# Kernel tuning notes

Measured on AMD Instinct MI355X. Metric: run time of the kernel, lower is better.

## Reference

```python
import jax, jax.numpy as jnp
import numpy as np
from jax import lax

DIM = 96
D_STATE = 16
D_CONV = 4
EXPAND = 2
D_INNER = EXPAND * DIM           # 192
DT_RANK = (DIM + 15) // 16       # 6
EPS = 1e-5


def _upsample2x_align_corners(x):
    # bilinear, align_corners=True, scale_factor=2 (matches nn.Upsample)
    B, C, H, W = x.shape
    def lin_idx(n_in, n_out):
        pos = jnp.arange(n_out) * ((n_in - 1) / (n_out - 1))
        i0 = jnp.floor(pos).astype(jnp.int32)
        i1 = jnp.minimum(i0 + 1, n_in - 1)
        w = (pos - i0).astype(x.dtype)
        return i0, i1, w
    r0, r1, rw = lin_idx(H, 2 * H)
    c0, c1, cw = lin_idx(W, 2 * W)
    xr = x[:, :, r0, :] * (1 - rw)[None, None, :, None] + x[:, :, r1, :] * rw[None, None, :, None]
    return xr[:, :, :, c0] * (1 - cw) + xr[:, :, :, c1] * cw


def _conv2d(x, w, b, pad):
    y = lax.conv_general_dilated(x, w, (1, 1), [(pad, pad), (pad, pad)],
                                 dimension_numbers=('NCHW', 'OIHW', 'NCHW'))
    return y + b[None, :, None, None]


def _instance_norm(x):
    m = x.mean(axis=(2, 3), keepdims=True)
    v = x.var(axis=(2, 3), keepdims=True)
    return (x - m) * lax.rsqrt(v + EPS)


def _selective_scan(u, dt, A, Bm, Cm, D):
    # u, dt: [B,L,Din]; Bm, Cm: [B,L,N]; A: [Din,N]; D: [Din]
    def step(h, inp):
        u_t, dt_t, B_t, C_t = inp                       # [B,Din],[B,Din],[B,N],[B,N]
        dA = jnp.exp(dt_t[..., None] * A)               # [B,Din,N]
        h = h * dA + (dt_t * u_t)[..., None] * B_t[:, None, :]
        y = jnp.einsum('bdn,bn->bd', h, C_t)
        return h, y
    Bsz, L, Din = u.shape
    h0 = jnp.zeros((Bsz, Din, A.shape[1]), u.dtype)
    xs = (u.swapaxes(0, 1), dt.swapaxes(0, 1), Bm.swapaxes(0, 1), Cm.swapaxes(0, 1))
    _, ys = lax.scan(step, h0, xs)                      # ys: [L,B,Din]
    return ys.swapaxes(0, 1) + u * D


def _mamba(xseq, in_proj_w, conv1d_w, conv1d_b, x_proj_w, dt_proj_w, dt_proj_b,
           A_log, D, out_proj_w):
    # xseq: [B,L,dim]
    xz = xseq @ in_proj_w.T                             # [B,L,2*Din]
    xin, z = jnp.split(xz, 2, axis=-1)
    xc = xin.swapaxes(1, 2)                             # [B,Din,L]
    xc = lax.conv_general_dilated(xc, conv1d_w, (1,), [(D_CONV - 1, 0)],
                                  dimension_numbers=('NCH', 'OIH', 'NCH'),
                                  feature_group_count=D_INNER)
    xc = xc + conv1d_b[None, :, None]
    u = jax.nn.silu(xc.swapaxes(1, 2))                  # [B,L,Din]
    x_dbl = u @ x_proj_w.T                              # [B,L,dt_rank+2N]
    dt, Bm, Cm = jnp.split(x_dbl, [DT_RANK, DT_RANK + D_STATE], axis=-1)
    dt = jax.nn.softplus(dt @ dt_proj_w.T + dt_proj_b)  # [B,L,Din]
    A = -jnp.exp(A_log)                                 # [Din,N]
    y = _selective_scan(u, dt, A, Bm, Cm, D)
    y = y * jax.nn.silu(z)
    return y @ out_proj_w.T                             # [B,L,dim]


def setup_inputs() -> dict:
    key = jax.random.key(0)
    ks = jax.random.split(key, 16)
    s = 0.05
    inp = {
        'x': jax.random.normal(ks[0], (2, DIM, 64, 64), jnp.float32),
        'Hx': jax.random.normal(ks[1], (2, DIM * 2, 128, 128), jnp.float32),
        'conv1_w': jax.random.normal(ks[2], (DIM, DIM * 3, 1, 1), jnp.float32) * s,
        'conv1_b': jax.random.normal(ks[3], (DIM,), jnp.float32) * s,
        'conv2_w': jax.random.normal(ks[4], (DIM, DIM, 3, 3), jnp.float32) * s,
        'conv2_b': jax.random.normal(ks[5], (DIM,), jnp.float32) * s,
        'conv3_w': jax.random.normal(ks[6], (DIM, DIM, 1, 1), jnp.float32) * s,
        'conv3_b': jax.random.normal(ks[7], (DIM,), jnp.float32) * s,
        'in_proj_w': jax.random.normal(ks[8], (2 * D_INNER, DIM), jnp.float32) * s,
        'conv1d_w': jax.random.normal(ks[9], (D_INNER, 1, D_CONV), jnp.float32) * s,
        'conv1d_b': jax.random.normal(ks[10], (D_INNER,), jnp.float32) * s,
        'x_proj_w': jax.random.normal(ks[11], (DT_RANK + 2 * D_STATE, D_INNER), jnp.float32) * s,
        'dt_proj_w': jax.random.normal(ks[12], (D_INNER, DT_RANK), jnp.float32) * s,
        'dt_proj_b': jax.random.normal(ks[13], (D_INNER,), jnp.float32) * 0.1,
        'A_log': jnp.log(jnp.tile(jnp.arange(1, D_STATE + 1, dtype=jnp.float32)[None, :], (D_INNER, 1))),
        'D': jnp.ones((D_INNER,), jnp.float32),
        'out_proj_w': jax.random.normal(ks[14], (DIM, D_INNER), jnp.float32) * s,
    }
    return inp


def reference(x, Hx, conv1_w, conv1_b, conv2_w, conv2_b, conv3_w, conv3_b,
              in_proj_w, conv1d_w, conv1d_b, x_proj_w, dt_proj_w, dt_proj_b,
              A_log, D, out_proj_w):
    up = _upsample2x_align_corners(x)                   # [B,dim,H,W]
    cat = jnp.concatenate([up, Hx], axis=1)             # [B,3*dim,H,W]
    h = _conv2d(cat, conv1_w, conv1_b, 0)
    h = _conv2d(h, conv2_w, conv2_b, 1)
    h = _conv2d(h, conv3_w, conv3_b, 0)
    Lx = jax.nn.selu(_instance_norm(h))                 # [B,dim,H,W]
    B, C, H, W = Lx.shape
    seq = Lx.reshape(B, C, H * W).swapaxes(1, 2)        # [B,L,dim]
    y = _mamba(seq, in_proj_w, conv1d_w, conv1d_b, x_proj_w, dt_proj_w,
               dt_proj_b, A_log, D, out_proj_w)
    return y.swapaxes(1, 2).reshape(B, C, H, W) + Lx
```

## Files before the change

kernel.cpp:

```cpp
#include <hip/hip_runtime.h>
#include <hip/hip_bf16.h>
#include <math.h>

#define LSEQ 16384
#define DIN  192
#define GCH  256
#define TCH  64

typedef float f4v __attribute__((ext_vector_type(4)));
typedef short s8v __attribute__((ext_vector_type(8)));
typedef unsigned short u16x8 __attribute__((ext_vector_type(8)));

__device__ __forceinline__ float siluf(float x) { return x / (1.0f + __expf(-x)); }
__device__ __forceinline__ unsigned short f2bf(float f) {
  unsigned int u = __float_as_uint(f);
  unsigned int r = (u + 0x7FFFu + ((u >> 16) & 1u)) >> 16;
  return (unsigned short)r;
}
__device__ __forceinline__ float bf2f(unsigned short s) {
  return __uint_as_float(((unsigned int)s) << 16);
}

__global__ __launch_bounds__(256) void k_packw(const float* __restrict__ c1w,
    const float* __restrict__ c2w, const float* __restrict__ c3w,
    const float* __restrict__ Win, const float* __restrict__ Wx,
    const float* __restrict__ Wout, unsigned short* __restrict__ P) {
  int i = blockIdx.x * 256 + threadIdx.x;
  if (i >= 184320) return;
  if (i < 27648) { P[i] = f2bf(c1w[i]); return; }
  int j = i - 27648;
  if (j < 82944) {
    int cc = j / 27648, r = j - cc * 27648;
    int kk = r / 3072, r2 = r - kk * 3072;
    int oc = r2 >> 5, icl = r2 & 31;
    int ky = kk / 3, kx = kk - ky * 3;
    P[i] = f2bf(c2w[((oc * 96 + cc * 32 + icl) * 3 + ky) * 3 + kx]);
    return;
  }
  j -= 82944;
  if (j < 9216) { P[i] = f2bf(c3w[j]); return; }
  j -= 9216;
  if (j < 36864) { P[i] = f2bf(Win[j]); return; }
  j -= 36864;
  if (j < 9216) {
    int oc = j / 192, k = j - oc * 192;
    P[i] = (oc < 38) ? f2bf(Wx[oc * 192 + k]) : (unsigned short)0;
    return;
  }
  j -= 9216;
  P[i] = f2bf(Wout[j]);
}

__global__ __launch_bounds__(256) void k_upsample(const float* __restrict__ x, float* __restrict__ up) {
  int idx = blockIdx.x * 256 + threadIdx.x;
  if (idx >= 2 * 96 * LSEQ) return;
  int ow = idx & 127, oh = (idx >> 7) & 127, bc = idx >> 14;
  float pr = oh * (63.0f / 127.0f); int r0 = (int)pr; float rw = pr - (float)r0; int r1 = min(r0 + 1, 63);
  float pc = ow * (63.0f / 127.0f); int c0 = (int)pc; float cw = pc - (float)c0; int c1 = min(c0 + 1, 63);
  const float* xp = x + (size_t)bc * 4096;
  float v00 = xp[r0 * 64 + c0], v01 = xp[r0 * 64 + c1];
  float v10 = xp[r1 * 64 + c0], v11 = xp[r1 * 64 + c1];
  float top = v00 + (v10 - v00) * rw;
  float bot = v01 + (v11 - v01) * rw;
  up[idx] = top + (bot - top) * cw;
}

#define SRC_PLANAR2 0
#define SRC_ROWS    1
#define OUT_BF16R    0
#define OUT_F32P     1
#define OUT_F32R     2
#define OUT_BF16RG   3
#define OUT_F32P_RES 4

template<int SM, int OM, int NT>
__global__ __launch_bounds__(256) void k_gemm(
    const void* __restrict__ xa, const void* __restrict__ xb, int CA,
    const unsigned short* __restrict__ Wp, const float* __restrict__ bias,
    void* __restrict__ outv, const float* __restrict__ resid,
    int K, int ostride, int oc0g, int ng) {
  __shared__ unsigned short x_t[128 * 96];
  __shared__ unsigned short w_t[NT * 16 * 96];
  Wp += (size_t)blockIdx.y * 96 * K;
  oc0g += blockIdx.y * 96;
  int pxg0 = blockIdx.x * 128;
  int b = pxg0 >> 14, px_in0 = pxg0 & 16383;
  int tid = threadIdx.x, lane = tid & 63, wv = tid >> 6;
  int r = lane & 15, q = lane >> 4;
  f4v acc[2][NT];
#pragma unroll
  for (int mi = 0; mi < 2; mi++)
#pragma unroll
    for (int n = 0; n < NT; n++) acc[mi][n] = (f4v)0.0f;
  int nchunk = K / 96;
  for (int kc = 0; kc < nchunk; kc++) {
    for (int t = tid; t < NT * 16 * 12; t += 256) {
      int row = t / 12, u8 = t - row * 12;
      *(u16x8*)&w_t[row * 96 + u8 * 8] = *(const u16x8*)&Wp[(size_t)row * K + kc * 96 + u8 * 8];
    }
    if (SM == SRC_PLANAR2) {
      const float* A0 = (const float*)xa;
      const float* A1 = (const float*)xb;
      int CB = K - CA;
      for (int t = tid; t < 3072; t += 256) {
        int px4 = t / 96, c_l = t - px4 * 96;
        int c = kc * 96 + c_l;
        const float* sp = (c < CA) ? (A0 + ((size_t)b * CA + c) * LSEQ + px_in0 + px4 * 4)
                                   : (A1 + ((size_t)b * CB + (c - CA)) * LSEQ + px_in0 + px4 * 4);
        float4 v = *(const float4*)sp;
        x_t[(px4 * 4 + 0) * 96 + c_l] = f2bf(v.x);
        x_t[(px4 * 4 + 1) * 96 + c_l] = f2bf(v.y);
        x_t[(px4 * 4 + 2) * 96 + c_l] = f2bf(v.z);
        x_t[(px4 * 4 + 3) * 96 + c_l] = f2bf(v.w);
      }
    } else {
      const unsigned short* X = (const unsigned short*)xa;
      for (int t = tid; t < 1536; t += 256) {
        int rr = t / 12, u8 = t - rr * 12;
        *(u16x8*)&x_t[rr * 96 + u8 * 8] =
            *(const u16x8*)&X[(size_t)(pxg0 + rr) * K + kc * 96 + u8 * 8];
      }
    }
    __syncthreads();
#pragma unroll
    for (int k0 = 0; k0 < 96; k0 += 32) {
      s8v a0 = *(const s8v*)&x_t[((wv * 2 + 0) * 16 + r) * 96 + k0 + q * 8];
      s8v a1 = *(const s8v*)&x_t[((wv * 2 + 1) * 16 + r) * 96 + k0 + q * 8];
#pragma unroll
      for (int n = 0; n < NT; n++) {
        s8v bb = *(const s8v*)&w_t[(n * 16 + r) * 96 + k0 + q * 8];
        acc[0][n] = __builtin_amdgcn_mfma_f32_16x16x32_bf16(a0, bb, acc[0][n], 0, 0, 0);
        acc[1][n] = __builtin_amdgcn_mfma_f32_16x16x32_bf16(a1, bb, acc[1][n], 0, 0, 0);
      }
    }
    __syncthreads();
  }
#pragma unroll
  for (int mi = 0; mi < 2; mi++) {
    int pxl = (wv * 2 + mi) * 16 + q * 4;
    int pxg = pxg0 + pxl;
#pragma unroll
    for (int n = 0; n < NT; n++) {
      int oc = n * 16 + r;
      if (OM == OUT_BF16R) {
        float bv = bias[oc];
        unsigned short* O = (unsigned short*)outv;
#pragma unroll
        for (int g = 0; g < 4; g++)
          O[(size_t)(pxg + g) * 96 + oc] = f2bf(acc[mi][n][g] + bv);
      } else if (OM == OUT_F32P) {
        float bv = bias[oc];
        float* O = (float*)outv;
        float4 o = make_float4(acc[mi][n][0] + bv, acc[mi][n][1] + bv,
                               acc[mi][n][2] + bv, acc[mi][n][3] + bv);
        *(float4*)&O[((size_t)b * 96 + oc) * LSEQ + px_in0 + pxl] = o;
      } else if (OM == OUT_F32P_RES) {
        float* O = (float*)outv;
        size_t ad = ((size_t)b * 96 + oc) * LSEQ + px_in0 + pxl;
        float4 rv = *(const float4*)&resid[ad];
        float4 o = make_float4(acc[mi][n][0] + rv.x, acc[mi][n][1] + rv.y,
                               acc[mi][n][2] + rv.z, acc[mi][n][3] + rv.w);
        *(float4*)&O[ad] = o;
      } else if (OM == OUT_F32R) {
        float* O = (float*)outv;
        int ocg = oc0g + oc;
        if (ocg < ng) {
#pragma unroll
          for (int g = 0; g < 4; g++)
            O[(size_t)(pxg + g) * ostride + ocg] = acc[mi][n][g];
        }
      } else {
        unsigned short* O = (unsigned short*)outv;
        int ocg = oc0g + oc;
#pragma unroll
        for (int g = 0; g < 4; g++)
          O[(size_t)(pxg + g) * ostride + ocg] = f2bf(acc[mi][n][g]);
      }
    }
  }
}

__global__ __launch_bounds__(256) void k_conv3x3m(const unsigned short* __restrict__ X,
    const unsigned short* __restrict__ Wp2, const float* __restrict__ bias,
    unsigned short* __restrict__ out) {
  __shared__ unsigned short in_t[3 * 68 * 32];
  __shared__ unsigned short w_t[9 * 96 * 32];
  int bi = blockIdx.x;
  int hx = bi & 1, y = (bi >> 1) & 127, b = bi >> 8;
  int px0 = hx * 64;
  int tid = threadIdx.x, lane = tid & 63, wv = tid >> 6;
  int r = lane & 15, q = lane >> 4;
  f4v acc[6];
#pragma unroll
  for (int n = 0; n < 6; n++) acc[n] = (f4v)0.0f;
  for (int cc = 0; cc < 3; cc++) {
    for (int t = tid; t < 3456; t += 256)
      *(u16x8*)&w_t[t * 8] = *(const u16x8*)&Wp2[cc * 27648 + t * 8];
    for (int t = tid; t < 792; t += 256) {
      int row = t / 264, rem = t - row * 264;
      int c_l = rem >> 2, icq = rem & 3;
      int gy = y - 1 + row, gx = px0 - 1 + c_l;
      u16x8 v = {0, 0, 0, 0, 0, 0, 0, 0};
      if (gy >= 0 && gy < 128 && gx >= 0 && gx < 128)
        v = *(const u16x8*)&X[(((size_t)b * 128 + gy) * 128 + gx) * 96 + cc * 32 + icq * 8];
      *(u16x8*)&in_t[(row * 68 + c_l) * 32 + icq * 8] = v;
    }
    __syncthreads();
#pragma unroll
    for (int kk = 0; kk < 9; kk++) {
      int ky = kk / 3, kx = kk - ky * 3;
      s8v a = *(const s8v*)&in_t[(ky * 68 + wv * 16 + r + kx) * 32 + q * 8];
#pragma unroll
      for (int n = 0; n < 6; n++) {
        s8v bb = *(const s8v*)&w_t[(kk * 96 + n * 16 + r) * 32 + q * 8];
        acc[n] = __builtin_amdgcn_mfma_f32_16x16x32_bf16(a, bb, acc[n], 0, 0, 0);
      }
    }
    __syncthreads();
  }
  size_t rowbase = ((size_t)b * 128 + y) * 128 + px0 + wv * 16 + q * 4;
#pragma unroll
  for (int n = 0; n < 6; n++) {
    int oc = n * 16 + r;
    float bv = bias[oc];
#pragma unroll
    for (int g = 0; g < 4; g++)
      out[(rowbase + g) * 96 + oc] = f2bf(acc[n][g] + bv);
  }
}

__global__ __launch_bounds__(256) void k_stats(const float* __restrict__ h, float* __restrict__ stats) {
  int bc = blockIdx.x;
  const float* p = h + (size_t)bc * LSEQ;
  float s = 0.f, ss = 0.f;
  for (int i = threadIdx.x; i < LSEQ; i += 256) { float v = p[i]; s += v; ss = fmaf(v, v, ss); }
  __shared__ float rs[256], rss[256];
  int tid = threadIdx.x;
  rs[tid] = s; rss[tid] = ss; __syncthreads();
  for (int o = 128; o > 0; o >>= 1) {
    if (tid < o) { rs[tid] += rs[tid + o]; rss[tid] += rss[tid + o]; }
    __syncthreads();
  }
  if (tid == 0) {
    float m = rs[0] * (1.0f / LSEQ);
    float var = rss[0] * (1.0f / LSEQ) - m * m;
    stats[bc * 2] = m;
    stats[bc * 2 + 1] = rsqrtf(fmaxf(var, 0.f) + 1e-5f);
  }
}

__global__ __launch_bounds__(256) void k_normselu2(const float* __restrict__ h,
    const float* __restrict__ stats, float* __restrict__ Lx, unsigned short* __restrict__ LxR) {
  __shared__ float tile[96 * 65];
  int px0 = blockIdx.x * 64, b = blockIdx.y;
  int tid = threadIdx.x;
  const float kS = 1.0507009873554805f, kA = 1.6732632423543772f;
  for (int t = tid; t < 1536; t += 256) {
    int c = t >> 4, p4 = t & 15;
    size_t ga = ((size_t)b * 96 + c) * LSEQ + px0 + p4 * 4;
    float4 v = *(const float4*)&h[ga];
    float m = stats[(b * 96 + c) * 2], rv = stats[(b * 96 + c) * 2 + 1];
    v.x = (v.x - m) * rv; v.y = (v.y - m) * rv; v.z = (v.z - m) * rv; v.w = (v.w - m) * rv;
    v.x = v.x > 0.f ? kS * v.x : kS * kA * expm1f(v.x);
    v.y = v.y > 0.f ? kS * v.y : kS * kA * expm1f(v.y);
    v.z = v.z > 0.f ? kS * v.z : kS * kA * expm1f(v.z);
    v.w = v.w > 0.f ? kS * v.w : kS * kA * expm1f(v.w);
    *(float4*)&Lx[ga] = v;
    tile[c * 65 + p4 * 4 + 0] = v.x;
    tile[c * 65 + p4 * 4 + 1] = v.y;
    tile[c * 65 + p4 * 4 + 2] = v.z;
    tile[c * 65 + p4 * 4 + 3] = v.w;
  }
  __syncthreads();
  for (int t = tid; t < 768; t += 256) {
    int px = t / 12, c8 = t - px * 12;
    u16x8 o;
#pragma unroll
    for (int jj = 0; jj < 8; jj++) o[jj] = f2bf(tile[(c8 * 8 + jj) * 65 + px]);
    *(u16x8*)&LxR[((size_t)b * LSEQ + px0 + px) * 96 + c8 * 8] = o;
  }
}

__global__ __launch_bounds__(256) void k_conv1d(const float* __restrict__ xzx,
    const float* __restrict__ w1d, const float* __restrict__ b1d,
    float* __restrict__ u, unsigned short* __restrict__ uR) {
  int gid = blockIdx.x * 256 + threadIdx.x;
  if (gid >= 2 * LSEQ * DIN) return;
  int d = gid % DIN, bl = gid / DIN;
  int l = bl & (LSEQ - 1);
  float4 w = *(const float4*)&w1d[d * 4];
  float wv[4] = {w.x, w.y, w.z, w.w};
  float acc = b1d[d];
#pragma unroll
  for (int k = 0; k < 4; k++) {
    int lk = l - 3 + k;
    if (lk >= 0) acc = fmaf(wv[k], xzx[(size_t)(bl - 3 + k) * DIN + d], acc);
  }
  float s = siluf(acc);
  u[gid] = s;
  uR[gid] = f2bf(s);
}

__global__ __launch_bounds__(256) void k_dtproj(const float* __restrict__ xdbl,
    const float* __restrict__ Wdt, const float* __restrict__ bdt, float* __restrict__ dt) {
  int gid = blockIdx.x * 256 + threadIdx.x;
  if (gid >= 2 * LSEQ * DIN) return;
  int d = gid % DIN, bl = gid / DIN;
  const float* xp = xdbl + (size_t)bl * 38;
  const float* wp = Wdt + d * 6;
  float acc = bdt[d];
#pragma unroll
  for (int r = 0; r < 6; r++) acc = fmaf(xp[r], wp[r], acc);
  dt[gid] = acc > 20.f ? acc : log1pf(__expf(acc));
}

__global__ __launch_bounds__(192) void k_scanA(const float* __restrict__ dt,
    const float* __restrict__ u, const float* __restrict__ xdbl,
    const float* __restrict__ Alog, float* __restrict__ chA, float* __restrict__ chB) {
  int b = blockIdx.y, g = blockIdx.x, d = threadIdx.x;
  __shared__ float Bs[TCH * 16];
  for (int i = threadIdx.x; i < TCH * 16; i += 192) {
    int t = i >> 4, n = i & 15;
    Bs[i] = xdbl[(size_t)(b * LSEQ + g * TCH + t) * 38 + 6 + n];
  }
  float ac[16];
#pragma unroll
  for (int n = 0; n < 16; n++) ac[n] = -__expf(Alog[d * 16 + n]);
  __syncthreads();
  float ap[16], hb[16];
#pragma unroll
  for (int n = 0; n < 16; n++) { ap[n] = 1.f; hb[n] = 0.f; }
  for (int t = 0; t < TCH; t++) {
    size_t base = (size_t)(b * LSEQ + g * TCH + t);
    float dtv = dt[base * DIN + d];
    float uv = u[base * DIN + d];
    float du = dtv * uv;
    float bs[16];
    const float4* src = (const float4*)&Bs[t * 16];
#pragma unroll
    for (int qq = 0; qq < 4; qq++) {
      float4 v = src[qq];
      bs[qq * 4] = v.x; bs[qq * 4 + 1] = v.y; bs[qq * 4 + 2] = v.z; bs[qq * 4 + 3] = v.w;
    }
#pragma unroll
    for (int n = 0; n < 16; n++) {
      float e = __expf(dtv * ac[n]);
      ap[n] *= e;
      hb[n] = fmaf(hb[n], e, du * bs[n]);
    }
  }
  size_t co = ((size_t)(b * GCH + g) * DIN + d) * 16;
#pragma unroll
  for (int qq = 0; qq < 4; qq++) {
    ((float4*)(chA + co))[qq] = make_float4(ap[qq * 4], ap[qq * 4 + 1], ap[qq * 4 + 2], ap[qq * 4 + 3]);
    ((float4*)(chB + co))[qq] = make_float4(hb[qq * 4], hb[qq * 4 + 1], hb[qq * 4 + 2], hb[qq * 4 + 3]);
  }
}

__global__ __launch_bounds__(256) void k_scanB(const float* __restrict__ chA,
    const float* __restrict__ chB, float* __restrict__ h0) {
  int tid = blockIdx.x * 256 + threadIdx.x;
  if (tid >= 2 * DIN * 16) return;
  int b = tid / (DIN * 16), rem = tid - b * DIN * 16;
  float h = 0.f;
#pragma unroll 4
  for (int g = 0; g < GCH; g++) {
    size_t off = (size_t)(b * GCH + g) * (DIN * 16) + rem;
    h0[off] = h;
    h = fmaf(h, chA[off], chB[off]);
  }
}

__global__ __launch_bounds__(192) void k_scanC(const float* __restrict__ dt,
    const float* __restrict__ u, const float* __restrict__ xdbl,
    const unsigned short* __restrict__ zR, const float* __restrict__ Alog,
    const float* __restrict__ Dp, const float* __restrict__ h0, unsigned short* __restrict__ yR) {
  int b = blockIdx.y, g = blockIdx.x, d = threadIdx.x;
  __shared__ float Bs[TCH * 16], Cs[TCH * 16];
  for (int i = threadIdx.x; i < TCH * 16; i += 192) {
    int t = i >> 4, n = i & 15;
    size_t rb = (size_t)(b * LSEQ + g * TCH + t) * 38;
    Bs[i] = xdbl[rb + 6 + n];
    Cs[i] = xdbl[rb + 22 + n];
  }
  float ac[16];
#pragma unroll
  for (int n = 0; n < 16; n++) ac[n] = -__expf(Alog[d * 16 + n]);
  float Dd = Dp[d];
  __syncthreads();
  size_t co = ((size_t)(b * GCH + g) * DIN + d) * 16;
  float h[16];
#pragma unroll
  for (int qq = 0; qq < 4; qq++) {
    float4 v = ((const float4*)(h0 + co))[qq];
    h[qq * 4] = v.x; h[qq * 4 + 1] = v.y; h[qq * 4 + 2] = v.z; h[qq * 4 + 3] = v.w;
  }
  for (int t = 0; t < TCH; t++) {
    size_t base = (size_t)(b * LSEQ + g * TCH + t);
    float dtv = dt[base * DIN + d];
    float uv = u[base * DIN + d];
    float zv = bf2f(zR[base * DIN + d]);
    float du = dtv * uv;
    float bs[16], cs[16];
    const float4* sb = (const float4*)&Bs[t * 16];
    const float4* sc = (const float4*)&Cs[t * 16];
#pragma unroll
    for (int qq = 0; qq < 4; qq++) {
      float4 vb = sb[qq], vc = sc[qq];
      bs[qq * 4] = vb.x; bs[qq * 4 + 1] = vb.y; bs[qq * 4 + 2] = vb.z; bs[qq * 4 + 3] = vb.w;
      cs[qq * 4] = vc.x; cs[qq * 4 + 1] = vc.y; cs[qq * 4 + 2] = vc.z; cs[qq * 4 + 3] = vc.w;
    }
    float y0 = 0.f, y1 = 0.f, y2 = 0.f, y3 = 0.f;
#pragma unroll
    for (int n = 0; n < 16; n++) {
      float e = __expf(dtv * ac[n]);
      h[n] = fmaf(h[n], e, du * bs[n]);
      float p = h[n] * cs[n];
      if ((n & 3) == 0) y0 += p; else if ((n & 3) == 1) y1 += p;
      else if ((n & 3) == 2) y2 += p; else y3 += p;
    }
    float yv = ((y0 + y1) + (y2 + y3)) + uv * Dd;
    yR[base * DIN + d] = f2bf(yv * siluf(zv));
  }
}

extern "C" void kernel_launch(void* const* d_in, const int* in_sizes, int n_in,
                              void* d_out, int out_size, void* d_ws, size_t ws_size,
                              hipStream_t stream) {
  (void)in_sizes; (void)n_in; (void)out_size; (void)ws_size;
  const float* x    = (const float*)d_in[0];
  const float* Hx   = (const float*)d_in[1];
  const float* c1w  = (const float*)d_in[2];
  const float* c1b  = (const float*)d_in[3];
  const float* c2w  = (const float*)d_in[4];
  const float* c2b  = (const float*)d_in[5];
  const float* c3w  = (const float*)d_in[6];
  const float* c3b  = (const float*)d_in[7];
  const float* Win  = (const float*)d_in[8];
  const float* w1d  = (const float*)d_in[9];
  const float* b1d  = (const float*)d_in[10];
  const float* Wx   = (const float*)d_in[11];
  const float* Wdt  = (const float*)d_in[12];
  const float* bdt  = (const float*)d_in[13];
  const float* Alog = (const float*)d_in[14];
  const float* Dp   = (const float*)d_in[15];
  const float* Wout = (const float*)d_in[16];
  float* out = (float*)d_out;

  float* ws = (float*)d_ws;
  const size_t F = (size_t)2 * 96 * LSEQ;
  const size_t Fh = F / 2;
  const size_t XDBL = (size_t)2 * LSEQ * 38;

  float*          b_up = ws;
  float*          b_h3 = ws;
  float*          chA  = ws;
  float*          chB  = ws + Fh;
  float*          b_Lx = ws + F;
  unsigned short* R1   = (unsigned short*)(ws + 2 * F);
  unsigned short* R2   = (unsigned short*)(ws + 2 * F + Fh);
  float*          h0b  = ws + 2 * F + Fh;
  float*          xzx  = ws + 3 * F;
  float*          b_dt = ws + 3 * F;
  unsigned short* zRb  = (unsigned short*)(ws + 5 * F);
  unsigned short* R3   = (unsigned short*)(ws + 6 * F);
  float*          b_u  = ws + 7 * F;
  float*          xdbl = ws + 9 * F;
  unsigned short* Wp   = (unsigned short*)(ws + 9 * F + XDBL);
  float*          b_st = ws + 9 * F + XDBL + 92160;

  k_packw<<<dim3(720), dim3(256), 0, stream>>>(c1w, c2w, c3w, Win, Wx, Wout, Wp);
  k_upsample<<<dim3(12288), dim3(256), 0, stream>>>(x, b_up);
  k_gemm<SRC_PLANAR2, OUT_BF16R, 6><<<dim3(256, 1), dim3(256), 0, stream>>>(
      b_up, Hx, 96, Wp, c1b, R1, nullptr, 288, 0, 0, 0);
  k_conv3x3m<<<dim3(512), dim3(256), 0, stream>>>(R1, Wp + 27648, c2b, R2);
  k_gemm<SRC_ROWS, OUT_F32P, 6><<<dim3(256, 1), dim3(256), 0, stream>>>(
      R2, nullptr, 0, Wp + 110592, c3b, b_h3, nullptr, 96, 0, 0, 0);
  k_stats<<<dim3(192), dim3(256), 0, stream>>>(b_h3, b_st);
  k_normselu2<<<dim3(256, 2), dim3(256), 0, stream>>>(b_h3, b_st, b_Lx, R1);
  k_gemm<SRC_ROWS, OUT_F32R, 6><<<dim3(256, 2), dim3(256), 0, stream>>>(
      R1, nullptr, 0, Wp + 119808, nullptr, xzx, nullptr, 96, 192, 0, 1 << 30);
  k_gemm<SRC_ROWS, OUT_BF16RG, 6><<<dim3(256, 2), dim3(256), 0, stream>>>(
      R1, nullptr, 0, Wp + 119808 + 192 * 96, nullptr, zRb, nullptr, 96, 192, 0, 0);
  k_conv1d<<<dim3((2 * LSEQ * DIN + 255) / 256), dim3(256), 0, stream>>>(xzx, w1d, b1d, b_u, R3);
  k_gemm<SRC_ROWS, OUT_F32R, 3><<<dim3(256, 1), dim3(256), 0, stream>>>(
      R3, nullptr, 0, Wp + 156672, nullptr, xdbl, nullptr, 192, 38, 0, 38);
  k_dtproj<<<dim3((2 * LSEQ * DIN + 255) / 256), dim3(256), 0, stream>>>(xdbl, Wdt, bdt, b_dt);
  k_scanA<<<dim3(GCH, 2), dim3(192), 0, stream>>>(b_dt, b_u, xdbl, Alog, chA, chB);
  k_scanB<<<dim3(24), dim3(256), 0, stream>>>(chA, chB, h0b);
  k_scanC<<<dim3(GCH, 2), dim3(192), 0, stream>>>(b_dt, b_u, xdbl, zRb, Alog, Dp, h0b, R3);
  k_gemm<SRC_ROWS, OUT_F32P_RES, 6><<<dim3(256, 1), dim3(256), 0, stream>>>(
      R3, nullptr, 0, Wp + 165888, nullptr, out, b_Lx, 192, 0, 0, 0);
}
```

Before: 411.3 us.

## Fuse dt projection into scan kernels, merge xz GEMMs, double scan chunks

```diff
diff --git a/kernel.cpp b/kernel.cpp
--- a/kernel.cpp
+++ b/kernel.cpp
@@ -4,8 +4,8 @@
 
 #define LSEQ 16384
 #define DIN  192
-#define GCH  256
-#define TCH  64
+#define GCH  512
+#define TCH  32
 
 typedef float f4v __attribute__((ext_vector_type(4)));
 typedef short s8v __attribute__((ext_vector_type(8)));
@@ -70,19 +70,18 @@
 #define OUT_BF16R    0
 #define OUT_F32P     1
 #define OUT_F32R     2
-#define OUT_BF16RG   3
 #define OUT_F32P_RES 4
+#define OUT_XZ       5
 
 template<int SM, int OM, int NT>
 __global__ __launch_bounds__(256) void k_gemm(
     const void* __restrict__ xa, const void* __restrict__ xb, int CA,
     const unsigned short* __restrict__ Wp, const float* __restrict__ bias,
-    void* __restrict__ outv, const float* __restrict__ resid,
-    int K, int ostride, int oc0g, int ng) {
+    void* __restrict__ outv, void* __restrict__ outv2, const float* __restrict__ resid,
+    int K, int ostride, int ng) {
   __shared__ unsigned short x_t[128 * 96];
   __shared__ unsigned short w_t[NT * 16 * 96];
   Wp += (size_t)blockIdx.y * 96 * K;
-  oc0g += blockIdx.y * 96;
   int pxg0 = blockIdx.x * 128;
   int b = pxg0 >> 14, px_in0 = pxg0 & 16383;
   int tid = threadIdx.x, lane = tid & 63, wv = tid >> 6;
@@ -163,18 +162,25 @@
         *(float4*)&O[ad] = o;
       } else if (OM == OUT_F32R) {
         float* O = (float*)outv;
-        int ocg = oc0g + oc;
+        int ocg = blockIdx.y * 96 + oc;
         if (ocg < ng) {
 #pragma unroll
           for (int g = 0; g < 4; g++)
             O[(size_t)(pxg + g) * ostride + ocg] = acc[mi][n][g];
         }
       } else {
-        unsigned short* O = (unsigned short*)outv;
-        int ocg = oc0g + oc;
-#pragma unroll
-        for (int g = 0; g < 4; g++)
-          O[(size_t)(pxg + g) * ostride + ocg] = f2bf(acc[mi][n][g]);
+        int ocg = (blockIdx.y & 1) * 96 + oc;
+        if (blockIdx.y < 2) {
+          float* O = (float*)outv;
+#pragma unroll
+          for (int g = 0; g < 4; g++)
+            O[(size_t)(pxg + g) * 192 + ocg] = acc[mi][n][g];
+        } else {
+          unsigned short* O = (unsigned short*)outv2;
+#pragma unroll
+          for (int g = 0; g < 4; g++)
+            O[(size_t)(pxg + g) * 192 + ocg] = f2bf(acc[mi][n][g]);
+        }
       }
     }
   }
@@ -301,39 +307,38 @@
   uR[gid] = f2bf(s);
 }
 
-__global__ __launch_bounds__(256) void k_dtproj(const float* __restrict__ xdbl,
-    const float* __restrict__ Wdt, const float* __restrict__ bdt, float* __restrict__ dt) {
-  int gid = blockIdx.x * 256 + threadIdx.x;
-  if (gid >= 2 * LSEQ * DIN) return;
-  int d = gid % DIN, bl = gid / DIN;
-  const float* xp = xdbl + (size_t)bl * 38;
-  const float* wp = Wdt + d * 6;
-  float acc = bdt[d];
-#pragma unroll
-  for (int r = 0; r < 6; r++) acc = fmaf(xp[r], wp[r], acc);
-  dt[gid] = acc > 20.f ? acc : log1pf(__expf(acc));
-}
-
-__global__ __launch_bounds__(192) void k_scanA(const float* __restrict__ dt,
-    const float* __restrict__ u, const float* __restrict__ xdbl,
-    const float* __restrict__ Alog, float* __restrict__ chA, float* __restrict__ chB) {
+__global__ __launch_bounds__(192) void k_scanA(const float* __restrict__ u,
+    const float* __restrict__ xdbl, const float* __restrict__ Wdt,
+    const float* __restrict__ bdt, const float* __restrict__ Alog,
+    float* __restrict__ chA, float* __restrict__ chB) {
   int b = blockIdx.y, g = blockIdx.x, d = threadIdx.x;
-  __shared__ float Bs[TCH * 16];
-  for (int i = threadIdx.x; i < TCH * 16; i += 192) {
+  __shared__ float Bs[TCH * 16], Dts[TCH * 8];
+  for (int i = d; i < TCH * 16; i += 192) {
     int t = i >> 4, n = i & 15;
     Bs[i] = xdbl[(size_t)(b * LSEQ + g * TCH + t) * 38 + 6 + n];
   }
+  for (int i = d; i < TCH * 6; i += 192) {
+    int t = i / 6, c = i - t * 6;
+    Dts[t * 8 + c] = xdbl[(size_t)(b * LSEQ + g * TCH + t) * 38 + c];
+  }
   float ac[16];
 #pragma unroll
   for (int n = 0; n < 16; n++) ac[n] = -__expf(Alog[d * 16 + n]);
+  float wdt[6];
+#pragma unroll
+  for (int c = 0; c < 6; c++) wdt[c] = Wdt[d * 6 + c];
+  float bd = bdt[d];
   __syncthreads();
   float ap[16], hb[16];
 #pragma unroll
   for (int n = 0; n < 16; n++) { ap[n] = 1.f; hb[n] = 0.f; }
   for (int t = 0; t < TCH; t++) {
     size_t base = (size_t)(b * LSEQ + g * TCH + t);
-    float dtv = dt[base * DIN + d];
     float uv = u[base * DIN + d];
+    float dtraw = bd;
+#pragma unroll
+    for (int c = 0; c < 6; c++) dtraw = fmaf(Dts[t * 8 + c], wdt[c], dtraw);
+    float dtv = dtraw > 20.f ? dtraw : log1pf(__expf(dtraw));
     float du = dtv * uv;
     float bs[16];
     const float4* src = (const float4*)&Bs[t * 16];
@@ -371,21 +376,30 @@
   }
 }
 
-__global__ __launch_bounds__(192) void k_scanC(const float* __restrict__ dt,
-    const float* __restrict__ u, const float* __restrict__ xdbl,
-    const unsigned short* __restrict__ zR, const float* __restrict__ Alog,
-    const float* __restrict__ Dp, const float* __restrict__ h0, unsigned short* __restrict__ yR) {
+__global__ __launch_bounds__(192) void k_scanC(const float* __restrict__ u,
+    const float* __restrict__ xdbl, const float* __restrict__ Wdt,
+    const float* __restrict__ bdt, const unsigned short* __restrict__ zR,
+    const float* __restrict__ Alog, const float* __restrict__ Dp,
+    const float* __restrict__ h0, unsigned short* __restrict__ yR) {
   int b = blockIdx.y, g = blockIdx.x, d = threadIdx.x;
-  __shared__ float Bs[TCH * 16], Cs[TCH * 16];
-  for (int i = threadIdx.x; i < TCH * 16; i += 192) {
+  __shared__ float Bs[TCH * 16], Cs[TCH * 16], Dts[TCH * 8];
+  for (int i = d; i < TCH * 16; i += 192) {
     int t = i >> 4, n = i & 15;
     size_t rb = (size_t)(b * LSEQ + g * TCH + t) * 38;
     Bs[i] = xdbl[rb + 6 + n];
     Cs[i] = xdbl[rb + 22 + n];
   }
+  for (int i = d; i < TCH * 6; i += 192) {
+    int t = i / 6, c = i - t * 6;
+    Dts[t * 8 + c] = xdbl[(size_t)(b * LSEQ + g * TCH + t) * 38 + c];
+  }
   float ac[16];
 #pragma unroll
   for (int n = 0; n < 16; n++) ac[n] = -__expf(Alog[d * 16 + n]);
+  float wdt[6];
+#pragma unroll
+  for (int c = 0; c < 6; c++) wdt[c] = Wdt[d * 6 + c];
+  float bd = bdt[d];
   float Dd = Dp[d];
   __syncthreads();
   size_t co = ((size_t)(b * GCH + g) * DIN + d) * 16;
@@ -397,9 +411,12 @@
   }
   for (int t = 0; t < TCH; t++) {
     size_t base = (size_t)(b * LSEQ + g * TCH + t);
-    float dtv = dt[base * DIN + d];
     float uv = u[base * DIN + d];
     float zv = bf2f(zR[base * DIN + d]);
+    float dtraw = bd;
+#pragma unroll
+    for (int c = 0; c < 6; c++) dtraw = fmaf(Dts[t * 8 + c], wdt[c], dtraw);
+    float dtv = dtraw > 20.f ? dtraw : log1pf(__expf(dtraw));
     float du = dtv * uv;
     float bs[16], cs[16];
     const float4* sb = (const float4*)&Bs[t * 16];
@@ -450,45 +467,40 @@
   float* ws = (float*)d_ws;
   const size_t F = (size_t)2 * 96 * LSEQ;
   const size_t Fh = F / 2;
-  const size_t XDBL = (size_t)2 * LSEQ * 38;
 
   float*          b_up = ws;
   float*          b_h3 = ws;
   float*          chA  = ws;
-  float*          chB  = ws + Fh;
   float*          b_Lx = ws + F;
   unsigned short* R1   = (unsigned short*)(ws + 2 * F);
   unsigned short* R2   = (unsigned short*)(ws + 2 * F + Fh);
-  float*          h0b  = ws + 2 * F + Fh;
+  float*          xdbl = ws + 2 * F + Fh;
   float*          xzx  = ws + 3 * F;
-  float*          b_dt = ws + 3 * F;
+  float*          chB  = ws + 3 * F;
+  float*          h0b  = ws + 4 * F;
   unsigned short* zRb  = (unsigned short*)(ws + 5 * F);
   unsigned short* R3   = (unsigned short*)(ws + 6 * F);
   float*          b_u  = ws + 7 * F;
-  float*          xdbl = ws + 9 * F;
-  unsigned short* Wp   = (unsigned short*)(ws + 9 * F + XDBL);
-  float*          b_st = ws + 9 * F + XDBL + 92160;
+  unsigned short* Wp   = (unsigned short*)(ws + 9 * F);
+  float*          b_st = ws + 9 * F + 92160;
 
   k_packw<<<dim3(720), dim3(256), 0, stream>>>(c1w, c2w, c3w, Win, Wx, Wout, Wp);
   k_upsample<<<dim3(12288), dim3(256), 0, stream>>>(x, b_up);
   k_gemm<SRC_PLANAR2, OUT_BF16R, 6><<<dim3(256, 1), dim3(256), 0, stream>>>(
-      b_up, Hx, 96, Wp, c1b, R1, nullptr, 288, 0, 0, 0);
+      b_up, Hx, 96, Wp, c1b, R1, nullptr, nullptr, 288, 0, 0);
   k_conv3x3m<<<dim3(512), dim3(256), 0, stream>>>(R1, Wp + 27648, c2b, R2);
   k_gemm<SRC_ROWS, OUT_F32P, 6><<<dim3(256, 1), dim3(256), 0, stream>>>(
-      R2, nullptr, 0, Wp + 110592, c3b, b_h3, nullptr, 96, 0, 0, 0);
+      R2, nullptr, 0, Wp + 110592, c3b, b_h3, nullptr, nullptr, 96, 0, 0);
   k_stats<<<dim3(192), dim3(256), 0, stream>>>(b_h3, b_st);
   k_normselu2<<<dim3(256, 2), dim3(256), 0, stream>>>(b_h3, b_st, b_Lx, R1);
-  k_gemm<SRC_ROWS, OUT_F32R, 6><<<dim3(256, 2), dim3(256), 0, stream>>>(
-      R1, nullptr, 0, Wp + 119808, nullptr, xzx, nullptr, 96, 192, 0, 1 << 30);
-  k_gemm<SRC_ROWS, OUT_BF16RG, 6><<<dim3(256, 2), dim3(256), 0, stream>>>(
-      R1, nullptr, 0, Wp + 119808 + 192 * 96, nullptr, zRb, nullptr, 96, 192, 0, 0);
+  k_gemm<SRC_ROWS, OUT_XZ, 6><<<dim3(256, 4), dim3(256), 0, stream>>>(
+      R1, nullptr, 0, Wp + 119808, nullptr, xzx, zRb, nullptr, 96, 192, 0);
   k_conv1d<<<dim3((2 * LSEQ * DIN + 255) / 256), dim3(256), 0, stream>>>(xzx, w1d, b1d, b_u, R3);
   k_gemm<SRC_ROWS, OUT_F32R, 3><<<dim3(256, 1), dim3(256), 0, stream>>>(
-      R3, nullptr, 0, Wp + 156672, nullptr, xdbl, nullptr, 192, 38, 0, 38);
-  k_dtproj<<<dim3((2 * LSEQ * DIN + 255) / 256), dim3(256), 0, stream>>>(xdbl, Wdt, bdt, b_dt);
-  k_scanA<<<dim3(GCH, 2), dim3(192), 0, stream>>>(b_dt, b_u, xdbl, Alog, chA, chB);
+      R3, nullptr, 0, Wp + 156672, nullptr, xdbl, nullptr, nullptr, 192, 38, 38);
+  k_scanA<<<dim3(GCH, 2), dim3(192), 0, stream>>>(b_u, xdbl, Wdt, bdt, Alog, chA, chB);
   k_scanB<<<dim3(24), dim3(256), 0, stream>>>(chA, chB, h0b);
-  k_scanC<<<dim3(GCH, 2), dim3(192), 0, stream>>>(b_dt, b_u, xdbl, zRb, Alog, Dp, h0b, R3);
+  k_scanC<<<dim3(GCH, 2), dim3(192), 0, stream>>>(b_u, xdbl, Wdt, bdt, zRb, Alog, Dp, h0b, R3);
   k_gemm<SRC_ROWS, OUT_F32P_RES, 6><<<dim3(256, 1), dim3(256), 0, stream>>>(
-      R3, nullptr, 0, Wp + 165888, nullptr, out, b_Lx, 192, 0, 0, 0);
-}
+      R3, nullptr, 0, Wp + 165888, nullptr, out, nullptr, b_Lx, 192, 0, 0);
+}
```

Measured after the change: 425.9 us. 1.04x slower.
